# Performance work log

Hardware: AMD Instinct MI355X
Metric: run time of the kernel (lower is better)

The kernel has to match this reference:

```python
import math
import jax, jax.numpy as jnp
import numpy as np

B, S, D = 8, 512, 1024        # batch, seq (dec and enc), model dim
HID, NH = 1024, 16            # attention hidden, heads
C = HID // NH                 # per-head channels (self-attn 'attends' over this dim!)
EPS = 1e-5


def setup_inputs() -> dict:
    key = jax.random.key(0)
    ks = jax.random.split(key, 26)
    w = lambda k, sh: (jax.random.normal(k, sh, jnp.float32) * 0.02)
    inp = {
        "x": jax.random.normal(ks[0], (B, S, D), jnp.float32),
        "h": jax.random.normal(ks[1], (B, S, D), jnp.float32),
        # self-attn (AttentionModule) params, stored [in, out]
        "Wq": w(ks[2], (D, HID)), "bq": jnp.zeros((HID,), jnp.float32),
        "Wk": w(ks[3], (D, HID)), "bk": jnp.zeros((HID,), jnp.float32),
        "Wv": w(ks[4], (D, HID)), "bv": jnp.zeros((HID,), jnp.float32),
        "Wo": w(ks[5], (HID, D)), "bo": jnp.zeros((D,), jnp.float32),
        # cross-attn params
        "Wcq": w(ks[6], (D, HID)), "bcq": jnp.zeros((HID,), jnp.float32),
        "Wck": w(ks[7], (D, HID)), "bck": jnp.zeros((HID,), jnp.float32),
        "Wcv": w(ks[8], (D, HID)), "bcv": jnp.zeros((HID,), jnp.float32),
        "Wco": w(ks[9], (HID, D)), "bco": jnp.zeros((D,), jnp.float32),
        "gamma": jnp.ones((D,), jnp.float32), "beta": jnp.zeros((D,), jnp.float32),
        # FFN (two Linears, NO nonlinearity, per original code)
        "W1": w(ks[10], (D, HID)), "b1": jnp.zeros((HID,), jnp.float32),
        "W2": w(ks[11], (HID, D)), "b2": jnp.zeros((D,), jnp.float32),
    }
    return inp


def _layernorm(x, gamma, beta):
    mu = jnp.mean(x, axis=-1, keepdims=True)
    var = jnp.mean(jnp.square(x - mu), axis=-1, keepdims=True)
    return (x - mu) * jax.lax.rsqrt(var + EPS) * gamma + beta


def _self_attn(x, Wq, bq, Wk, bk, Wv, bv, Wo, bo):
    # FAITHFUL to original: reshape [B,S,NH,C]; einsum '...hq,...hk->...hqk' with
    # batch dims [B,S] -> attention over the C channel dim per token, causal mask over channels.
    Q = (x @ Wq + bq).reshape(B, S, NH, C) / math.sqrt(C)
    K = (x @ Wk + bk).reshape(B, S, NH, C)
    V = (x @ Wv + bv).reshape(B, S, NH, C)
    aff = jnp.einsum('bshq,bshk->bshqk', Q, K)            # [B,S,NH,C,C]
    mask = jnp.triu(jnp.full((C, C), -jnp.inf, jnp.float32), k=1)  # -inf above diag, 0 else
    aff = aff + mask
    w = jax.nn.softmax(aff, axis=-1)
    av = jnp.einsum('bshqk,bshk->bshq', w, V)             # [B,S,NH,C]
    return av.reshape(B, S, HID) @ Wo + bo


def _cross_attn(xd, he, Wcq, bcq, Wck, bck, Wcv, bcv, Wco, bco):
    # standard multi-head cross attention, but scaled by sqrt(d_full) per original
    Q = (xd @ Wcq + bcq).reshape(B, S, NH, C).transpose(0, 2, 1, 3)  # [B,NH,Sq,C]
    K = (he @ Wck + bck).reshape(B, S, NH, C).transpose(0, 2, 1, 3)
    V = (he @ Wcv + bcv).reshape(B, S, NH, C).transpose(0, 2, 1, 3)
    scores = jnp.einsum('bhqd,bhkd->bhqk', Q, K) / math.sqrt(HID)
    p = jax.nn.softmax(scores, axis=-1)
    o = jnp.einsum('bhqk,bhkd->bhqd', p, V)               # [B,NH,Sq,C]
    o = o.transpose(0, 2, 1, 3).reshape(B, S, HID)
    return o @ Wco + bco


def reference(x, h, Wq, bq, Wk, bk, Wv, bv, Wo, bo,
              Wcq, bcq, Wck, bck, Wcv, bcv, Wco, bco,
              gamma, beta, W1, b1, W2, b2):
    out = _self_attn(x, Wq, bq, Wk, bk, Wv, bv, Wo, bo) + x
    out = _layernorm(out, gamma, beta)
    out = _cross_attn(out, h, Wcq, bcq, Wck, bck, Wcv, bcv, Wco, bco) + out
    out = _layernorm(out, gamma, beta)
    out = ((out @ W1 + b1) @ W2 + b2) + out
    out = _layernorm(out, gamma, beta)
    return out
```

## Files before the change

### kernel.cpp

```cpp
#include <hip/hip_runtime.h>

typedef __bf16 bf16_t;
typedef bf16_t bf16x8 __attribute__((ext_vector_type(8)));
typedef bf16_t bf16x4 __attribute__((ext_vector_type(4)));
typedef float f32x4 __attribute__((ext_vector_type(4)));
typedef unsigned u32x4 __attribute__((ext_vector_type(4)));

__device__ __forceinline__ void async_copy16(const void* g, void* l) {
  __builtin_amdgcn_global_load_lds(
      (const __attribute__((address_space(1))) unsigned int*)(unsigned long long)g,
      (__attribute__((address_space(3))) unsigned int*)(unsigned int)(unsigned long long)l,
      16, 0, 0);
}

__device__ __forceinline__ float fast_exp2(float x) {
#if __has_builtin(__builtin_amdgcn_exp2f)
  return __builtin_amdgcn_exp2f(x);
#else
  float r;
  asm volatile("v_exp_f32 %0, %1\n\ts_nop 0" : "=v"(r) : "v"(x));
  return r;
#endif
}
__device__ __forceinline__ float fast_rcp(float x) {
#if __has_builtin(__builtin_amdgcn_rcpf)
  return __builtin_amdgcn_rcpf(x);
#else
  float r;
  asm volatile("v_rcp_f32 %0, %1\n\ts_nop 0" : "=v"(r) : "v"(x));
  return r;
#endif
}

__device__ __forceinline__ unsigned pack_bf16(float x, float y) {
  bf16_t lo = (bf16_t)x, hi = (bf16_t)y;
  unsigned short ul, uh;
  __builtin_memcpy(&ul, &lo, 2);
  __builtin_memcpy(&uh, &hi, 2);
  return (unsigned)ul | ((unsigned)uh << 16);
}

#define QSCALE 0.180336688f

struct SrcPtrs { const float* p[10]; };
__global__ __launch_bounds__(256) void prep_main(
    SrcPtrs srcs, bf16_t* __restrict__ dstbase,
    const float* __restrict__ a, const float* __restrict__ b,
    const float* __restrict__ w1, bf16_t* __restrict__ dst1,
    bf16_t* __restrict__ dstw) {
  __shared__ float tile[32][33];
  int bid = blockIdx.x;
  int tid = threadIdx.x;
  if (bid < 10240) {
    int z = bid >> 10;
    int rem = bid & 1023;
    const float* src = srcs.p[z];
    bf16_t* dst = dstbase + (size_t)z * 1048576;
    float scale = (z == 0) ? QSCALE : ((z == 4) ? 0.03125f : 1.f);
    int bx = (rem & 31) * 32;
    int by = (rem >> 5) * 32;
    int tx = tid & 31, ty = tid >> 5;
#pragma unroll
    for (int i = 0; i < 32; i += 8)
      tile[ty + i][tx] = src[(size_t)(by + ty + i) * 1024 + bx + tx];
    __syncthreads();
#pragma unroll
    for (int i = 0; i < 32; i += 8)
      dst[(size_t)(bx + ty + i) * 1024 + by + tx] = (bf16_t)(tile[tx][ty + i] * scale);
  } else {
    int i = ((bid - 10240) * 256 + tid) * 8;
    const float* s;
    bf16_t* d;
    if (i < 4194304) { s = a + i; d = dst1 + i; }
    else if (i < 8388608) { s = b + i - 4194304; d = dst1 + i; }
    else { s = w1 + i - 8388608; d = dstw + (i - 8388608); }
    float4 u = *(const float4*)s;
    float4 v = *(const float4*)(s + 4);
    bf16x8 o;
    o[0]=(bf16_t)u.x; o[1]=(bf16_t)u.y; o[2]=(bf16_t)u.z; o[3]=(bf16_t)u.w;
    o[4]=(bf16_t)v.x; o[5]=(bf16_t)v.y; o[6]=(bf16_t)v.z; o[7]=(bf16_t)v.w;
    *(bf16x8*)d = o;
  }
}

__global__ __launch_bounds__(256) void prep_bias_kernel(
    const float* __restrict__ bq, const float* __restrict__ bk,
    const float* __restrict__ bv, const float* __restrict__ bck,
    const float* __restrict__ bcv, const float* __restrict__ bcq,
    const bf16_t* __restrict__ wt9, const float* __restrict__ b1,
    const float* __restrict__ b2, float* __restrict__ cb,
    float* __restrict__ cb2) {
  int bid = blockIdx.x;
  if (bid < 28) {
    int i = bid * 256 + threadIdx.x;
    if (i < 1024) cb[i] = bq[i] * QSCALE;
    else if (i < 2048) cb[i] = bk[i - 1024];
    else if (i < 3072) cb[i] = bv[i - 2048];
    else if (i < 4096) cb[i] = bck[i - 3072];
    else if (i < 5120) cb[i] = bcv[i - 4096];
    else if (i < 6144) cb[i] = bcq[i - 5120] * 0.03125f;
    else cb[i] = 0.f;
  } else {
    int n = (bid - 28) * 256 + threadIdx.x;
    const bf16_t* row = wt9 + (size_t)n * 1024;
    float acc = 0.f;
#pragma unroll 4
    for (int h = 0; h < 1024; h += 8) {
      bf16x8 v = *(const bf16x8*)(row + h);
      float4 ba = *(const float4*)(b1 + h);
      float4 bb = *(const float4*)(b1 + h + 4);
      acc += ba.x*(float)v[0] + ba.y*(float)v[1] + ba.z*(float)v[2] + ba.w*(float)v[3]
           + bb.x*(float)v[4] + bb.y*(float)v[5] + bb.z*(float)v[6] + bb.w*(float)v[7];
    }
    cb2[n] = acc + b2[n];
  }
}

template <int BN, int MI, bool HAS_RES, bool TRANS_OUT, bool DBUF>
__device__ __forceinline__ void gemm_core(
    const bf16_t* __restrict__ A, const bf16_t* __restrict__ Bt,
    const float* __restrict__ bias, const bf16_t* __restrict__ res,
    bf16_t* __restrict__ C, int ldC, int bm, int bn,
    bf16_t* As, bf16_t* Bs) {
  constexpr int NI = 4;
  constexpr int ASZ = 128 * 64, BSZ = BN * 64;
  int tid = threadIdx.x;
  int w = tid >> 6, lane = tid & 63;
  int fm = lane & 15, fq = lane >> 4;
  int wm = (BN == 128) ? (w >> 1) * 64 : w * 32;
  int wn = (BN == 128) ? (w & 1) * 64 : 0;
  f32x4 acc[MI][NI] = {};

  auto stage = [&](int kt, int half) {
    bf16_t* Ad = DBUF ? As + half * ASZ : As;
    bf16_t* Bd = DBUF ? Bs + half * BSZ : Bs;
#pragma unroll
    for (int i = 0; i < 4; i++) {
      int c = i * 256 + tid;
      int row = c >> 3, skg = (c & 7) ^ (row & 7);
      async_copy16(A + (size_t)(bm + row) * 1024 + kt + skg * 8, &Ad[c * 8]);
    }
#pragma unroll
    for (int i = 0; i < BN / 32; i++) {
      int c = i * 256 + tid;
      int row = c >> 3, skg = (c & 7) ^ (row & 7);
      async_copy16(Bt + (size_t)(bn + row) * 1024 + kt + skg * 8, &Bd[c * 8]);
    }
  };
  auto compute = [&](int half) {
    const bf16_t* Ac = DBUF ? As + half * ASZ : As;
    const bf16_t* Bc = DBUF ? Bs + half * BSZ : Bs;
#pragma unroll
    for (int ks = 0; ks < 2; ks++) {
      bf16x8 af[MI], bfr[NI];
      int kg = ks * 4 + fq;
#pragma unroll
      for (int mi = 0; mi < MI; mi++) {
        int row = wm + mi * 16 + fm;
        af[mi] = *(const bf16x8*)&Ac[row * 64 + ((kg ^ (row & 7)) * 8)];
      }
#pragma unroll
      for (int ni = 0; ni < NI; ni++) {
        int row = wn + ni * 16 + fm;
        bfr[ni] = *(const bf16x8*)&Bc[row * 64 + ((kg ^ (row & 7)) * 8)];
      }
#pragma unroll
      for (int mi = 0; mi < MI; mi++)
#pragma unroll
        for (int ni = 0; ni < NI; ni++)
          acc[mi][ni] = __builtin_amdgcn_mfma_f32_16x16x32_bf16(
              af[mi], bfr[ni], acc[mi][ni], 0, 0, 0);
    }
  };

  if (DBUF) {
    stage(0, 0);
    __syncthreads();
#pragma unroll
    for (int t = 0; t < 16; t++) {
      if (t < 15) stage((t + 1) * 64, (t + 1) & 1);
      compute(t & 1);
      __syncthreads();
    }
  } else {
    for (int kt = 0; kt < 1024; kt += 64) {
      stage(kt, 0);
      __syncthreads();
      compute(0);
      __syncthreads();
    }
  }

#pragma unroll
  for (int mi = 0; mi < MI; mi++) {
#pragma unroll
    for (int ni = 0; ni < NI; ni++) {
      int col = bn + wn + ni * 16 + fm;
      float bv = bias[col];
      if (TRANS_OUT) {
        int rowb = bm + wm + mi * 16 + fq * 4;
        bf16x4 w4;
#pragma unroll
        for (int r = 0; r < 4; r++) w4[r] = (bf16_t)(acc[mi][ni][r] + bv);
        *(bf16x4*)&C[(size_t)col * ldC + rowb] = w4;
      } else {
#pragma unroll
        for (int r = 0; r < 4; r++) {
          int row = bm + wm + mi * 16 + fq * 4 + r;
          float v = acc[mi][ni][r] + bv;
          if (HAS_RES) v += (float)res[(size_t)row * ldC + col];
          C[(size_t)row * ldC + col] = (bf16_t)v;
        }
      }
    }
  }
}

template <int GX, int GY, int BN>
__device__ __forceinline__ void xcd_map(int lin, int& bm, int& bn) {
  constexpr int HX = GX / 2, QY = GY / 4;
  int xcd = lin & 7, idx = lin >> 3;
  int ly = idx / HX, lx = idx - ly * HX;
  bm = ((xcd >> 1) * QY + ly) * 128;
  bn = ((xcd & 1) * HX + lx) * BN;
}

template <bool HAS_RES, bool TRANS_OUT>
__global__ __launch_bounds__(256) void gemm_bf16(
    const bf16_t* __restrict__ A, const bf16_t* __restrict__ Bt,
    const float* __restrict__ bias, const bf16_t* __restrict__ res,
    bf16_t* __restrict__ C, int ldC) {
  __shared__ bf16_t As[2 * 128 * 64];
  __shared__ bf16_t Bs[2 * 64 * 64];
  int bm, bn;
  xcd_map<16, 32, 64>(blockIdx.x + 16 * blockIdx.y, bm, bn);
  gemm_core<64, 2, HAS_RES, TRANS_OUT, true>(A, Bt, bias, res, C, ldC, bm, bn, As, Bs);
}

__global__ __launch_bounds__(256) void gemm_qkv_p(
    const bf16_t* __restrict__ xb, const bf16_t* __restrict__ wt0,
    const bf16_t* __restrict__ wt9, const bf16_t* __restrict__ w1bf,
    const float* __restrict__ cb, bf16_t* __restrict__ qkv,
    bf16_t* __restrict__ pt) {
  __shared__ bf16_t smem[2 * 128 * 64];
  int bid = blockIdx.x;
  if (bid >= 128) {
    int bm, bn;
    xcd_map<24, 32, 128>(bid - 128, bm, bn);
    gemm_core<128, 4, false, false, false>(xb, wt0, cb, nullptr, qkv, 3072,
                                           bm, bn, smem, smem + 128 * 64);
  } else {
    gemm_core<64, 2, false, false, false>(wt9, w1bf, cb + 6144, nullptr, pt, 1024,
                                          (bid >> 4) * 128, (bid & 15) * 64,
                                          smem, smem + 128 * 64);
  }
}

__global__ __launch_bounds__(256) void kvproj_selfattn(
    const bf16_t* __restrict__ hb, const bf16_t* __restrict__ wt4,
    const float* __restrict__ cb, bf16_t* __restrict__ kbuf,
    bf16_t* __restrict__ vt, const bf16_t* __restrict__ QKV,
    bf16_t* __restrict__ O) {
  __shared__ bf16_t As[128 * 64];
  __shared__ bf16_t Bs[64 * 64];
  int bid = blockIdx.x;
  if (bid < 1024) {
    int xcd = bid & 7, idx = bid >> 3;
    int ly = idx >> 4, lx = idx & 15;
    int bm = ((xcd >> 1) * 8 + ly) * 128;
    int region = 1 + (xcd & 1);
    int bn = lx * 64;
    const bf16_t* Bt = wt4 + (size_t)region * 1048576;
    if (region == 2) {
      gemm_core<64, 2, false, true, false>(hb, Bt, cb + 4096, nullptr, vt, 4096,
                                           bm, bn, As, Bs);
    } else {
      gemm_core<64, 2, false, false, false>(hb, Bt, cb + 3072, nullptr, kbuf, 1024,
                                            bm, bn, As, Bs);
    }
    return;
  }
  int tid = threadIdx.x;
  int lane = tid & 63;
  int unit = __builtin_amdgcn_readfirstlane((bid - 1024) * 4 + (tid >> 6));
  int m = unit >> 4, h = unit & 15;
  size_t base = (size_t)m * 3072 + h * 64;
  size_t iq = base + lane;
  float qv = (float)QKV[iq];
  float kown = (float)QKV[iq + 1024];
  float vown = (float)QKV[iq + 2048];
  const u32x4* Krow = (const u32x4*)(QKV + base + 1024);
  const u32x4* Vrow = (const u32x4*)(QKV + base + 2048);
  u32x4 K4[8], V4[8];
#pragma unroll
  for (int i = 0; i < 8; i++) { K4[i] = Krow[i]; V4[i] = Vrow[i]; }
  float l0 = 0.f, l1 = 0.f, o0 = 0.f, o1 = 0.f;
#pragma unroll
  for (int p = 0; p < 32; p++) {
    unsigned kw = K4[p >> 2][p & 3];
    unsigned vw = V4[p >> 2][p & 3];
    float k0 = __uint_as_float(kw << 16);
    float k1 = __uint_as_float(kw & 0xffff0000u);
    float v0 = __uint_as_float(vw << 16);
    float v1 = __uint_as_float(vw & 0xffff0000u);
    float e0 = fast_exp2(qv * k0);
    float e1 = fast_exp2(qv * k1);
    bool c = lane >= 2 * p + 1;
    e0 = c ? e0 : 0.f;
    e1 = c ? e1 : 0.f;
    l0 += e0; o0 = fmaf(e0, v0, o0);
    l1 += e1; o1 = fmaf(e1, v1, o1);
  }
  float ed = fast_exp2(qv * kown);
  ed = ((lane & 1) == 0) ? ed : 0.f;
  float l = (l0 + l1) + ed;
  float o = fmaf(ed, vown, o0 + o1);
  O[(size_t)m * 1024 + h * 64 + lane] = (bf16_t)(o * fast_rcp(l));
}

__global__ __launch_bounds__(256) void cross_attn_mfma(
    const bf16_t* __restrict__ Q, const bf16_t* __restrict__ Kb,
    const bf16_t* __restrict__ Vt, bf16_t* __restrict__ O) {
  __shared__ bf16_t Ks[64 * 64];
  __shared__ bf16_t Vs[64 * 64];
  int tid = threadIdx.x;
  int w = tid >> 6, lane = tid & 63;
  int fm = lane & 15, fq = lane >> 4;
  int bh = blockIdx.x;
  int b = bh >> 4, h = bh & 15;
  int q0 = blockIdx.y * 64 + w * 16;
  const bf16_t* Qp = Q + (size_t)(b * 512 + q0 + fm) * 1024 + h * 64 + fq * 8;
  bf16x8 qf0 = *(const bf16x8*)Qp;
  bf16x8 qf1 = *(const bf16x8*)(Qp + 32);
  f32x4 o[4] = {};
  float mx = -1e30f, l = 0.f;
  for (int k0 = 0; k0 < 512; k0 += 64) {
    __syncthreads();
#pragma unroll
    for (int i = 0; i < 2; i++) {
      int c = i * 256 + tid;
      int row = c >> 3, kg = (c & 7) ^ (row & 7);
      async_copy16(Kb + (size_t)(b * 512 + k0 + row) * 1024 + h * 64 + kg * 8,
                   &Ks[c * 8]);
      async_copy16(Vt + (size_t)(h * 64 + row) * 4096 + b * 512 + k0 + kg * 8,
                   &Vs[c * 8]);
    }
    __syncthreads();
    f32x4 s[4] = {};
#pragma unroll
    for (int mt = 0; mt < 4; mt++) {
      int row = mt * 16 + fm;
#pragma unroll
      for (int f = 0; f < 2; f++) {
        int kg = f * 4 + fq;
        bf16x8 kf = *(const bf16x8*)&Ks[row * 64 + ((kg ^ (row & 7)) * 8)];
        s[mt] = __builtin_amdgcn_mfma_f32_16x16x32_bf16(
            kf, (f ? qf1 : qf0), s[mt], 0, 0, 0);
      }
    }
    float smax = -1e30f;
#pragma unroll
    for (int mt = 0; mt < 4; mt++)
#pragma unroll
      for (int r = 0; r < 4; r++) smax = fmaxf(smax, s[mt][r]);
    smax = fmaxf(smax, __shfl_xor(smax, 16, 64));
    smax = fmaxf(smax, __shfl_xor(smax, 32, 64));
    float nm = fmaxf(mx, smax);
    float corr = __expf(mx - nm);
    float ladd = 0.f;
    unsigned pk0[4], pk1[4];
#pragma unroll
    for (int mt = 0; mt < 4; mt++) {
      float p0 = __expf(s[mt][0] - nm);
      float p1 = __expf(s[mt][1] - nm);
      float p2 = __expf(s[mt][2] - nm);
      float p3 = __expf(s[mt][3] - nm);
      ladd += (p0 + p1) + (p2 + p3);
      pk0[mt] = pack_bf16(p0, p1);
      pk1[mt] = pack_bf16(p2, p3);
    }
    ladd += __shfl_xor(ladd, 16, 64);
    ladd += __shfl_xor(ladd, 32, 64);
    l = l * corr + ladd;
#pragma unroll
    for (int ct = 0; ct < 4; ct++)
#pragma unroll
      for (int r = 0; r < 4; r++) o[ct][r] *= corr;
    union U { unsigned u[4]; bf16x8 v; } pf[2];
    int sl0 = ((fq & 1) * 2) * 16 + fm;
    int sl1 = sl0 + 16;
    bool hi = fq >= 2;
#pragma unroll
    for (int f = 0; f < 2; f++) {
      unsigned a0 = (unsigned)__shfl((int)pk0[f * 2],     sl0, 64);
      unsigned b0 = (unsigned)__shfl((int)pk0[f * 2 + 1], sl0, 64);
      unsigned a1 = (unsigned)__shfl((int)pk1[f * 2],     sl0, 64);
      unsigned b1 = (unsigned)__shfl((int)pk1[f * 2 + 1], sl0, 64);
      unsigned a2 = (unsigned)__shfl((int)pk0[f * 2],     sl1, 64);
      unsigned b2 = (unsigned)__shfl((int)pk0[f * 2 + 1], sl1, 64);
      unsigned a3 = (unsigned)__shfl((int)pk1[f * 2],     sl1, 64);
      unsigned b3 = (unsigned)__shfl((int)pk1[f * 2 + 1], sl1, 64);
      pf[f].u[0] = hi ? b0 : a0;
      pf[f].u[1] = hi ? b1 : a1;
      pf[f].u[2] = hi ? b2 : a2;
      pf[f].u[3] = hi ? b3 : a3;
    }
#pragma unroll
    for (int ct = 0; ct < 4; ct++) {
      int row = ct * 16 + fm;
#pragma unroll
      for (int f = 0; f < 2; f++) {
        int kg = f * 4 + fq;
        bf16x8 vf = *(const bf16x8*)&Vs[row * 64 + ((kg ^ (row & 7)) * 8)];
        o[ct] = __builtin_amdgcn_mfma_f32_16x16x32_bf16(vf, pf[f].v, o[ct], 0, 0, 0);
      }
    }
    mx = nm;
  }
  float inv = 1.f / l;
  bf16_t* Op = O + (size_t)(b * 512 + q0 + fm) * 1024 + h * 64 + fq * 4;
#pragma unroll
  for (int ct = 0; ct < 4; ct++) {
    bf16x4 w4;
    w4[0] = (bf16_t)(o[ct][0] * inv);
    w4[1] = (bf16_t)(o[ct][1] * inv);
    w4[2] = (bf16_t)(o[ct][2] * inv);
    w4[3] = (bf16_t)(o[ct][3] * inv);
    *(bf16x4*)(Op + ct * 16) = w4;
  }
}

template <typename OutT>
__global__ __launch_bounds__(256) void ln_kernel(
    const bf16_t* __restrict__ X, const float* __restrict__ gamma,
    const float* __restrict__ beta, OutT* __restrict__ Y) {
  __shared__ float red[8];
  int row = blockIdx.x;
  int tid = threadIdx.x;
  bf16x4 x4 = *(const bf16x4*)(X + (size_t)row * 1024 + tid * 4);
  float4 v = {(float)x4[0], (float)x4[1], (float)x4[2], (float)x4[3]};
  float s = (v.x + v.y) + (v.z + v.w);
  float ss = fmaf(v.x, v.x, fmaf(v.y, v.y, fmaf(v.z, v.z, v.w * v.w)));
#pragma unroll
  for (int off = 32; off > 0; off >>= 1) {
    s  += __shfl_down(s, off, 64);
    ss += __shfl_down(ss, off, 64);
  }
  if ((tid & 63) == 0) { red[tid >> 6] = s; red[4 + (tid >> 6)] = ss; }
  __syncthreads();
  float S  = (red[0] + red[1]) + (red[2] + red[3]);
  float SS = (red[4] + red[5]) + (red[6] + red[7]);
  float mu = S * (1.f / 1024.f);
  float var = SS * (1.f / 1024.f) - mu * mu;
  float inv = rsqrtf(var + 1e-5f);
  float4 g = *(const float4*)(gamma + tid * 4);
  float4 b = *(const float4*)(beta + tid * 4);
  float r0 = (v.x - mu) * inv * g.x + b.x;
  float r1 = (v.y - mu) * inv * g.y + b.y;
  float r2 = (v.z - mu) * inv * g.z + b.z;
  float r3 = (v.w - mu) * inv * g.w + b.w;
  OutT* yp = Y + (size_t)row * 1024 + tid * 4;
  yp[0] = (OutT)r0; yp[1] = (OutT)r1; yp[2] = (OutT)r2; yp[3] = (OutT)r3;
}

extern "C" void kernel_launch(void* const* d_in, const int* in_sizes, int n_in,
                              void* d_out, int out_size, void* d_ws, size_t ws_size,
                              hipStream_t stream) {
  (void)in_sizes; (void)n_in; (void)out_size; (void)ws_size;
  const float* x  = (const float*)d_in[0];
  const float* hh = (const float*)d_in[1];
  SrcPtrs sp;
  sp.p[0] = (const float*)d_in[2];  sp.p[1] = (const float*)d_in[4];
  sp.p[2] = (const float*)d_in[6];  sp.p[3] = (const float*)d_in[8];
  sp.p[4] = (const float*)d_in[10]; sp.p[5] = (const float*)d_in[12];
  sp.p[6] = (const float*)d_in[14]; sp.p[7] = (const float*)d_in[16];
  sp.p[8] = (const float*)d_in[20]; sp.p[9] = (const float*)d_in[22];
  const float* W1f = (const float*)d_in[20];
  const float* bq  = (const float*)d_in[3];
  const float* bk  = (const float*)d_in[5];
  const float* bv  = (const float*)d_in[7];
  const float* bo  = (const float*)d_in[9];
  const float* bck = (const float*)d_in[13];
  const float* bcv = (const float*)d_in[15];
  const float* bcq = (const float*)d_in[11];
  const float* bco = (const float*)d_in[17];
  const float* gamma = (const float*)d_in[18];
  const float* beta  = (const float*)d_in[19];
  const float* b1  = (const float*)d_in[21];
  const float* b2  = (const float*)d_in[23];
  float* out = (float*)d_out;
  char* ws = (char*)d_ws;
  const size_t MB = 1048576;

  bf16_t* wt[10];
  for (int i = 0; i < 10; i++) wt[i] = (bf16_t*)(ws + (size_t)i * 2 * MB);
  float* cb      = (float*)(ws + 20 * MB);
  float* cb2     = (float*)(ws + 20 * MB + 32768);
  bf16_t* xb     = (bf16_t*)(ws + 21 * MB);
  bf16_t* hb     = (bf16_t*)(ws + 29 * MB);
  bf16_t* qkv    = (bf16_t*)(ws + 37 * MB);
  bf16_t* cqbuf  = (bf16_t*)(ws + 37 * MB);
  bf16_t* g4     = (bf16_t*)(ws + 45 * MB);
  bf16_t* kbuf   = (bf16_t*)(ws + 61 * MB);
  bf16_t* vtbuf  = (bf16_t*)(ws + 69 * MB);
  bf16_t* attn   = (bf16_t*)(ws + 77 * MB);
  bf16_t* ptbuf  = (bf16_t*)(ws + 85 * MB);
  bf16_t* w1bf   = (bf16_t*)(ws + 87 * MB);
  bf16_t* t1n    = xb;
  bf16_t* t2n    = hb;
  bf16_t* f2out  = g4;

  prep_main<<<14848, 256, 0, stream>>>(sp, (bf16_t*)ws, x, hh, W1f, xb, w1bf);
  prep_bias_kernel<<<32, 256, 0, stream>>>(bq, bk, bv, bck, bcv, bcq,
                                           wt[9], b1, b2, cb, cb2);

  gemm_qkv_p<<<896, 256, 0, stream>>>(xb, wt[0], wt[9], w1bf, cb, qkv, ptbuf);
  kvproj_selfattn<<<17408, 256, 0, stream>>>(hb, wt[4], cb, kbuf, vtbuf, qkv, attn);
  gemm_bf16<true, false><<<dim3(16, 32), 256, 0, stream>>>(attn, wt[3], bo, xb, g4, 1024);
  ln_kernel<bf16_t><<<4096, 256, 0, stream>>>(g4, gamma, beta, t1n);
  gemm_bf16<false, false><<<dim3(16, 32), 256, 0, stream>>>(t1n, wt[4], cb + 5120,
                                                            nullptr, cqbuf, 1024);
  cross_attn_mfma<<<dim3(128, 8), 256, 0, stream>>>(cqbuf, kbuf, vtbuf, attn);
  gemm_bf16<true, false><<<dim3(16, 32), 256, 0, stream>>>(attn, wt[7], bco, t1n, g4, 1024);
  ln_kernel<bf16_t><<<4096, 256, 0, stream>>>(g4, gamma, beta, t2n);
  gemm_bf16<true, false><<<dim3(16, 32), 256, 0, stream>>>(t2n, ptbuf, cb2, t2n, f2out, 1024);
  ln_kernel<float><<<4096, 256, 0, stream>>>(f2out, gamma, beta, out);
}
```

Before: 375.8 us.

## Interleave smaller KV-projection GEMM tiles with self-attention blocks in fused kernel

The fused K/V projection plus channel-attention kernel used to run 1024 GEMM blocks of 128x64 tiles first and then the attention blocks. Now every ninth block is a GEMM block with a 64x64 tile and a simple single-buffered inline MFMA loop with swizzled LDS, and the other eight are attention units. The goal is to spread the memory-bound attention work and the compute-bound GEMM work evenly across the CUs so they overlap, and to cut LDS use. In exchange, the smaller tiles reload operands more often, the K output is written as scalar stores, and the XCD-aware tile mapping is lost.

New measurement: 360.3 us. 1.04x faster.

```diff
diff --git a/kernel.cpp b/kernel.cpp
--- a/kernel.cpp
+++ b/kernel.cpp
@@ -261,28 +261,68 @@
     const float* __restrict__ cb, bf16_t* __restrict__ kbuf,
     bf16_t* __restrict__ vt, const bf16_t* __restrict__ QKV,
     bf16_t* __restrict__ O) {
-  __shared__ bf16_t As[128 * 64];
+  __shared__ bf16_t As[64 * 64];
   __shared__ bf16_t Bs[64 * 64];
   int bid = blockIdx.x;
-  if (bid < 1024) {
-    int xcd = bid & 7, idx = bid >> 3;
-    int ly = idx >> 4, lx = idx & 15;
-    int bm = ((xcd >> 1) * 8 + ly) * 128;
-    int region = 1 + (xcd & 1);
-    int bn = lx * 64;
-    const bf16_t* Bt = wt4 + (size_t)region * 1048576;
-    if (region == 2) {
-      gemm_core<64, 2, false, true, false>(hb, Bt, cb + 4096, nullptr, vt, 4096,
-                                           bm, bn, As, Bs);
-    } else {
-      gemm_core<64, 2, false, false, false>(hb, Bt, cb + 3072, nullptr, kbuf, 1024,
-                                            bm, bn, As, Bs);
+  int gsel = bid / 9;
+  int rem = bid - gsel * 9;
+  int tid = threadIdx.x;
+  if (rem == 8) {
+    int reg = gsel & 1;
+    int idx = gsel >> 1;
+    int bm = (idx & 63) * 64;
+    int bn = (idx >> 6) * 64;
+    const bf16_t* Bt = wt4 + (size_t)(1 + reg) * 1048576;
+    const float* bias = cb + (reg ? 4096 : 3072);
+    int w = tid >> 6, lane = tid & 63;
+    int fm = lane & 15, fq = lane >> 4;
+    int wm = w * 16;
+    f32x4 acc[4] = {};
+    for (int kt = 0; kt < 1024; kt += 64) {
+#pragma unroll
+      for (int i = 0; i < 2; i++) {
+        int c = i * 256 + tid;
+        int row = c >> 3, skg = (c & 7) ^ (row & 7);
+        async_copy16(hb + (size_t)(bm + row) * 1024 + kt + skg * 8, &As[c * 8]);
+        async_copy16(Bt + (size_t)(bn + row) * 1024 + kt + skg * 8, &Bs[c * 8]);
+      }
+      __syncthreads();
+#pragma unroll
+      for (int ks = 0; ks < 2; ks++) {
+        int kg = ks * 4 + fq;
+        int arow = wm + fm;
+        bf16x8 af = *(const bf16x8*)&As[arow * 64 + ((kg ^ (arow & 7)) * 8)];
+#pragma unroll
+        for (int ni = 0; ni < 4; ni++) {
+          int brow = ni * 16 + fm;
+          bf16x8 bfr = *(const bf16x8*)&Bs[brow * 64 + ((kg ^ (brow & 7)) * 8)];
+          acc[ni] = __builtin_amdgcn_mfma_f32_16x16x32_bf16(af, bfr, acc[ni], 0, 0, 0);
+        }
+      }
+      __syncthreads();
+    }
+#pragma unroll
+    for (int ni = 0; ni < 4; ni++) {
+      int col = bn + ni * 16 + fm;
+      float bv = bias[col];
+      if (reg) {
+        int rowb = bm + wm + fq * 4;
+        bf16x4 w4;
+#pragma unroll
+        for (int r = 0; r < 4; r++) w4[r] = (bf16_t)(acc[ni][r] + bv);
+        *(bf16x4*)&vt[(size_t)col * 4096 + rowb] = w4;
+      } else {
+#pragma unroll
+        for (int r = 0; r < 4; r++) {
+          int row = bm + wm + fq * 4 + r;
+          kbuf[(size_t)row * 1024 + col] = (bf16_t)(acc[ni][r] + bv);
+        }
+      }
     }
     return;
   }
-  int tid = threadIdx.x;
   int lane = tid & 63;
-  int unit = __builtin_amdgcn_readfirstlane((bid - 1024) * 4 + (tid >> 6));
+  int unit = __builtin_amdgcn_readfirstlane((gsel * 8 + rem) * 4 + (tid >> 6));
   int m = unit >> 4, h = unit & 15;
   size_t base = (size_t)m * 3072 + h * 64;
   size_t iq = base + lane;
@@ -515,7 +555,7 @@
                                            wt[9], b1, b2, cb, cb2);
 
   gemm_qkv_p<<<896, 256, 0, stream>>>(xb, wt[0], wt[9], w1bf, cb, qkv, ptbuf);
-  kvproj_selfattn<<<17408, 256, 0, stream>>>(hb, wt[4], cb, kbuf, vtbuf, qkv, attn);
+  kvproj_selfattn<<<18432, 256, 0, stream>>>(hb, wt[4], cb, kbuf, vtbuf, qkv, attn);
   gemm_bf16<true, false><<<dim3(16, 32), 256, 0, stream>>>(attn, wt[3], bo, xb, g4, 1024);
   ln_kernel<bf16_t><<<4096, 256, 0, stream>>>(g4, gamma, beta, t1n);
   gemm_bf16<false, false><<<dim3(16, 32), 256, 0, stream>>>(t1n, wt[4], cb + 5120,
```

## Move cross-attn K/V projection GEMMs into the QKV GEMM launch

Applied to the files above, without the earlier changes.

The K and V projections of the encoder states move out of the kernel that also ran self-attention and into one combined GEMM launch with the QKV and FFN-weight-product GEMMs. Self-attention becomes its own kernel. The intent is to pack all independent GEMM tiles into one wider launch for better CU fill, and to keep the memory-bound self-attention blocks from sharing a launch with GEMM tiles. The cost is that the K/V GEMMs no longer overlap with self-attention, and the different tile shapes in one grid may leave the load uneven across blocks.

New measurement: 369.2 us. No clear change (-1.7%).

```diff
diff --git a/kernel.cpp b/kernel.cpp
--- a/kernel.cpp
+++ b/kernel.cpp
@@ -237,52 +237,43 @@
   gemm_core<64, 2, HAS_RES, TRANS_OUT, true>(A, Bt, bias, res, C, ldC, bm, bn, As, Bs);
 }
 
-__global__ __launch_bounds__(256) void gemm_qkv_p(
+__global__ __launch_bounds__(256) void gemm_mega(
     const bf16_t* __restrict__ xb, const bf16_t* __restrict__ wt0,
     const bf16_t* __restrict__ wt9, const bf16_t* __restrict__ w1bf,
+    const bf16_t* __restrict__ hb, const bf16_t* __restrict__ wt4,
     const float* __restrict__ cb, bf16_t* __restrict__ qkv,
-    bf16_t* __restrict__ pt) {
+    bf16_t* __restrict__ pt, bf16_t* __restrict__ kbuf,
+    bf16_t* __restrict__ vt) {
   __shared__ bf16_t smem[2 * 128 * 64];
   int bid = blockIdx.x;
-  if (bid >= 128) {
+  if (bid < 768) {
     int bm, bn;
-    xcd_map<24, 32, 128>(bid - 128, bm, bn);
+    xcd_map<24, 32, 128>(bid, bm, bn);
     gemm_core<128, 4, false, false, false>(xb, wt0, cb, nullptr, qkv, 3072,
                                            bm, bn, smem, smem + 128 * 64);
+  } else if (bid < 896) {
+    int idx = bid - 768;
+    gemm_core<64, 2, false, false, false>(wt9, w1bf, cb + 6144, nullptr, pt, 1024,
+                                          (idx >> 4) * 128, (idx & 15) * 64,
+                                          smem, smem + 128 * 64);
+  } else if (bid < 1408) {
+    int bm, bn;
+    xcd_map<16, 32, 64>(bid - 896, bm, bn);
+    gemm_core<64, 2, false, false, false>(hb, wt4 + 1048576, cb + 3072, nullptr,
+                                          kbuf, 1024, bm, bn, smem, smem + 128 * 64);
   } else {
-    gemm_core<64, 2, false, false, false>(wt9, w1bf, cb + 6144, nullptr, pt, 1024,
-                                          (bid >> 4) * 128, (bid & 15) * 64,
-                                          smem, smem + 128 * 64);
-  }
-}
-
-__global__ __launch_bounds__(256) void kvproj_selfattn(
-    const bf16_t* __restrict__ hb, const bf16_t* __restrict__ wt4,
-    const float* __restrict__ cb, bf16_t* __restrict__ kbuf,
-    bf16_t* __restrict__ vt, const bf16_t* __restrict__ QKV,
-    bf16_t* __restrict__ O) {
-  __shared__ bf16_t As[128 * 64];
-  __shared__ bf16_t Bs[64 * 64];
-  int bid = blockIdx.x;
-  if (bid < 1024) {
-    int xcd = bid & 7, idx = bid >> 3;
-    int ly = idx >> 4, lx = idx & 15;
-    int bm = ((xcd >> 1) * 8 + ly) * 128;
-    int region = 1 + (xcd & 1);
-    int bn = lx * 64;
-    const bf16_t* Bt = wt4 + (size_t)region * 1048576;
-    if (region == 2) {
-      gemm_core<64, 2, false, true, false>(hb, Bt, cb + 4096, nullptr, vt, 4096,
-                                           bm, bn, As, Bs);
-    } else {
-      gemm_core<64, 2, false, false, false>(hb, Bt, cb + 3072, nullptr, kbuf, 1024,
-                                            bm, bn, As, Bs);
-    }
-    return;
-  }
+    int bm, bn;
+    xcd_map<16, 32, 64>(bid - 1408, bm, bn);
+    gemm_core<64, 2, false, true, false>(hb, wt4 + 2097152, cb + 4096, nullptr,
+                                         vt, 4096, bm, bn, smem, smem + 128 * 64);
+  }
+}
+
+__global__ __launch_bounds__(256) void self_attn_kernel(
+    const bf16_t* __restrict__ QKV, bf16_t* __restrict__ O) {
   int tid = threadIdx.x;
   int lane = tid & 63;
-  int unit = __builtin_amdgcn_readfirstlane((bid - 1024) * 4 + (tid >> 6));
+  int unit = __builtin_amdgcn_readfirstlane(blockIdx.x * 4 + (tid >> 6));
   int m = unit >> 4, h = unit & 15;
   size_t base = (size_t)m * 3072 + h * 64;
   size_t iq = base + lane;
@@ -514,8 +505,9 @@
   prep_bias_kernel<<<32, 256, 0, stream>>>(bq, bk, bv, bck, bcv, bcq,
                                            wt[9], b1, b2, cb, cb2);
 
-  gemm_qkv_p<<<896, 256, 0, stream>>>(xb, wt[0], wt[9], w1bf, cb, qkv, ptbuf);
-  kvproj_selfattn<<<17408, 256, 0, stream>>>(hb, wt[4], cb, kbuf, vtbuf, qkv, attn);
+  gemm_mega<<<1920, 256, 0, stream>>>(xb, wt[0], wt[9], w1bf, hb, wt[4], cb,
+                                      qkv, ptbuf, kbuf, vtbuf);
+  self_attn_kernel<<<16384, 256, 0, stream>>>(qkv, attn);
   gemm_bf16<true, false><<<dim3(16, 32), 256, 0, stream>>>(attn, wt[3], bo, xb, g4, 1024);
   ln_kernel<bf16_t><<<4096, 256, 0, stream>>>(g4, gamma, beta, t1n);
   gemm_bf16<false, false><<<dim3(16, 32), 256, 0, stream>>>(t1n, wt[4], cb + 5120,
```
